# Kernel optimization log

Measured on AMD Instinct MI355X. Metric: run time of the kernel, lower is better.

## Reference

```python
import jax, jax.numpy as jnp
import numpy as np

MEMORY_SIZE = 8192
FEATURE_DIM = 512
NUM_QUERIES = 32768
EPS = 1e-12  # guard for sqrt in cdist


def setup_inputs() -> dict:
    key = jax.random.key(0)
    k1, k2, k3, k4 = jax.random.split(key, 4)
    return {
        "features": jax.random.normal(k1, (MEMORY_SIZE, FEATURE_DIM), dtype=jnp.float32),
        "positions": jax.random.normal(k2, (MEMORY_SIZE, 3), dtype=jnp.float32),
        "query_positions": jax.random.normal(k3, (NUM_QUERIES, 3), dtype=jnp.float32),
        "position_embeddings": jax.random.normal(k4, (MEMORY_SIZE, 3), dtype=jnp.float32),
    }


def _cdist(a, b):
    # Euclidean distance via ||a||^2 + ||b||^2 - 2 a.b; avoids [Q,M,3] intermediate.
    a2 = jnp.sum(a * a, axis=-1, keepdims=True)          # [Q,1]
    b2 = jnp.sum(b * b, axis=-1, keepdims=True).T        # [1,M]
    d2 = a2 + b2 - 2.0 * (a @ b.T)                       # [Q,M]
    return jnp.sqrt(jnp.maximum(d2, EPS))


def reference(features, positions, query_positions, position_embeddings):
    # --- update ---
    positions_norm = positions / jnp.linalg.norm(positions, axis=-1, keepdims=True)
    embeddings_norm = position_embeddings / jnp.linalg.norm(position_embeddings, axis=-1, keepdims=True)
    sim = positions_norm @ embeddings_norm.T             # [M,M]
    attn = jax.nn.softmax(sim, axis=-1)
    memory = attn @ features                              # [M,F]
    new_pos_emb = attn @ positions                        # [M,3]
    # --- query ---
    dist = _cdist(query_positions, new_pos_emb)           # [Q,M]
    qattn = jax.nn.softmax(-dist, axis=-1)
    retrieved = qattn @ memory                            # [Q,F]
    return retrieved
```

## Files before the change

### kernel.cpp

```cpp
#include <hip/hip_runtime.h>
#include <stdint.h>
#include <stddef.h>

#define M_SZ 8192
#define F_DIM 512
#define N_Q 32768

typedef __attribute__((ext_vector_type(4))) float f32x4;
typedef __attribute__((ext_vector_type(8))) __bf16 bf16x8;

__device__ __forceinline__ unsigned bfround_bits(float x) {
    union { float f; unsigned u; } v; v.f = x;
    return (v.u + 0x7fffu + ((v.u >> 16) & 1u)) & 0xffff0000u;
}
__device__ __forceinline__ float bits_to_f(unsigned u) {
    union { unsigned u; float f; } v; v.u = u; return v.f;
}
__device__ __forceinline__ unsigned short f2bf(float x) {
    return (unsigned short)(bfround_bits(x) >> 16);
}

__global__ void prep_kernel(const float* __restrict__ pos,
                            const float* __restrict__ emb,
                            float* __restrict__ pn4,
                            float* __restrict__ en4,
                            float* __restrict__ pos4) {
    int i = blockIdx.x * 256 + threadIdx.x;
    if (i >= M_SZ) return;
    float x = pos[i * 3 + 0], y = pos[i * 3 + 1], z = pos[i * 3 + 2];
    float inv = 1.0f / __builtin_amdgcn_sqrtf(x * x + y * y + z * z);
    pn4[i * 4 + 0] = x * inv; pn4[i * 4 + 1] = y * inv;
    pn4[i * 4 + 2] = z * inv; pn4[i * 4 + 3] = 0.0f;
    pos4[i * 4 + 0] = x; pos4[i * 4 + 1] = y;
    pos4[i * 4 + 2] = z; pos4[i * 4 + 3] = 0.0f;
    float ex = emb[i * 3 + 0], ey = emb[i * 3 + 1], ez = emb[i * 3 + 2];
    float einv = 1.0f / __builtin_amdgcn_sqrtf(ex * ex + ey * ey + ez * ez);
    en4[i * 4 + 0] = ex * einv; en4[i * 4 + 1] = ey * einv;
    en4[i * 4 + 2] = ez * einv; en4[i * 4 + 3] = 0.0f;
}

__global__ void transpose_kernel(const float* __restrict__ feat,
                                 unsigned short* __restrict__ featT) {
    __shared__ float tile[64 * 65];
    const int jb = blockIdx.x * 64, fb = blockIdx.y * 64;
    const int t = threadIdx.x;
#pragma unroll
    for (int p = 0; p < 16; ++p) {
        int idx = p * 256 + t;
        int j = idx >> 6, f = idx & 63;
        tile[j * 65 + f] = feat[(size_t)(jb + j) * F_DIM + fb + f];
    }
    __syncthreads();
#pragma unroll
    for (int p = 0; p < 16; ++p) {
        int idx = p * 256 + t;
        int f = idx >> 6, j = idx & 63;
        featT[(size_t)(fb + f) * M_SZ + jb + j] = f2bf(tile[j * 65 + f]);
    }
}

__launch_bounds__(256, 3)
__global__ void build_memory_kernel(const float* __restrict__ pn4,
                                    const float* __restrict__ en4,
                                    const float* __restrict__ pos4,
                                    const unsigned short* __restrict__ featT,
                                    unsigned short* __restrict__ memT,
                                    float* __restrict__ npe4) {
    constexpr int BM = 64, BN = 256, BK = 32;
    constexpr int PSTR = BK + 8;
    __shared__ unsigned short pbuf[BM * PSTR];
    __shared__ unsigned short vbuf[BN * PSTR];
    __shared__ f32x4 etile[BK];
    __shared__ f32x4 ptile[BK];
    __shared__ f32x4 red[256];
    __shared__ float lbuf[BM];

    const int t = threadIdx.x;
    const int lane = t & 63, wv = t >> 6;
    const int mb = blockIdx.x * BM, fb = blockIdx.y * BN;
    const int r = t & 63, jq = t >> 6;

    const f32x4 pnr = ((const f32x4*)pn4)[mb + r];

    f32x4 acc[4][4];
    const f32x4 zero4 = {0.f, 0.f, 0.f, 0.f};
#pragma unroll
    for (int m = 0; m < 4; ++m)
#pragma unroll
        for (int n = 0; n < 4; ++n) acc[m][n] = zero4;
    float nx = 0.f, ny = 0.f, nz = 0.f, lp = 0.f;

    const unsigned short* vsrc = featT + (size_t)(fb + t) * M_SZ;

    for (int kt = 0; kt < M_SZ / BK; ++kt) {
        const int jb2 = kt * BK;
        __syncthreads();
        if (t < BK) etile[t] = ((const f32x4*)en4)[jb2 + t];
        else if (t < 2 * BK) ptile[t - BK] = ((const f32x4*)pos4)[jb2 + t - BK];
        const uint4* g = (const uint4*)(vsrc + jb2);
        uint4 v0 = g[0], v1 = g[1], v2 = g[2], v3 = g[3];
        __syncthreads();

        unsigned pk[4];
#pragma unroll
        for (int i = 0; i < 8; i += 2) {
            int j = jq * 8 + i;
            f32x4 e0 = etile[j], e1 = etile[j + 1];
            float s0 = fmaf(pnr.x, e0.x, fmaf(pnr.y, e0.y, pnr.z * e0.z));
            float s1 = fmaf(pnr.x, e1.x, fmaf(pnr.y, e1.y, pnr.z * e1.z));
            unsigned b0 = bfround_bits(__builtin_amdgcn_exp2f(s0 * 1.44269504f));
            unsigned b1 = bfround_bits(__builtin_amdgcn_exp2f(s1 * 1.44269504f));
            float w0 = bits_to_f(b0), w1 = bits_to_f(b1);
            f32x4 p0 = ptile[j], p1 = ptile[j + 1];
            lp += w0 + w1;
            nx = fmaf(w0, p0.x, fmaf(w1, p1.x, nx));
            ny = fmaf(w0, p0.y, fmaf(w1, p1.y, ny));
            nz = fmaf(w0, p0.z, fmaf(w1, p1.z, nz));
            pk[i >> 1] = (b0 >> 16) | (b1 & 0xffff0000u);
        }
        *(uint4*)(pbuf + r * PSTR + jq * 8) = make_uint4(pk[0], pk[1], pk[2], pk[3]);
        uint4* vd = (uint4*)(vbuf + t * PSTR);
        vd[0] = v0; vd[1] = v1; vd[2] = v2; vd[3] = v3;
        __syncthreads();

        const int col = lane & 15, quad = lane >> 4;
        bf16x8 a[4];
#pragma unroll
        for (int m = 0; m < 4; ++m)
            a[m] = *(const bf16x8*)(pbuf + (m * 16 + col) * PSTR + quad * 8);
#pragma unroll
        for (int n = 0; n < 4; ++n) {
            bf16x8 b = *(const bf16x8*)(vbuf + ((wv * 4 + n) * 16 + col) * PSTR + quad * 8);
#pragma unroll
            for (int m = 0; m < 4; ++m)
                acc[m][n] = __builtin_amdgcn_mfma_f32_16x16x32_bf16(a[m], b, acc[m][n], 0, 0, 0);
        }
    }

    f32x4 mine = {nx, ny, nz, lp};
    red[t] = mine;
    __syncthreads();
    if (t < BM) {
        f32x4 s = red[t];
        f32x4 s1 = red[t + 64], s2 = red[t + 128], s3 = red[t + 192];
        s.x += s1.x + s2.x + s3.x;
        s.y += s1.y + s2.y + s3.y;
        s.z += s1.z + s2.z + s3.z;
        s.w += s1.w + s2.w + s3.w;
        lbuf[t] = s.w;
        if (blockIdx.y == 0) {
            float inv = 1.0f / s.w;
            float X = s.x * inv, Y = s.y * inv, Z = s.z * inv;
            f32x4 o = {X, Y, Z, X * X + Y * Y + Z * Z};
            ((f32x4*)npe4)[mb + t] = o;
        }
    }
    __syncthreads();

    const int col = lane & 15, quad = lane >> 4;
#pragma unroll
    for (int m = 0; m < 4; ++m) {
        f32x4 l4 = *(const f32x4*)(lbuf + m * 16 + quad * 4);
        f32x4 inv4 = {1.0f / l4.x, 1.0f / l4.y, 1.0f / l4.z, 1.0f / l4.w};
        int mg = mb + m * 16 + quad * 4;
#pragma unroll
        for (int n = 0; n < 4; ++n) {
            int fg = fb + (wv * 4 + n) * 16 + col;
            ushort4 o;
            o.x = f2bf(acc[m][n].x * inv4.x);
            o.y = f2bf(acc[m][n].y * inv4.y);
            o.z = f2bf(acc[m][n].z * inv4.z);
            o.w = f2bf(acc[m][n].w * inv4.w);
            *(ushort4*)(memT + (size_t)fg * M_SZ + mg) = o;
        }
    }
}

__launch_bounds__(256, 2)
__global__ void query_kernel(const float* __restrict__ qpos,
                             const float* __restrict__ npe4,
                             const unsigned short* __restrict__ memT,
                             float* __restrict__ out) {
    constexpr int BM = 128, BN = 256, BK = 32;
    constexpr int PSTR = BK + 8;
    __shared__ unsigned short pbuf[BM * PSTR];
    __shared__ unsigned short vbuf[BN * PSTR];
    __shared__ f32x4 ntile[BK];
    __shared__ float red[256];
    __shared__ float lbuf[BM];

    const int t = threadIdx.x;
    const int lane = t & 63, wv = t >> 6;
    const int qb = blockIdx.x * BM, fb = blockIdx.y * BN;
    const int r = t & 127, jh = t >> 7;

    const float qx = qpos[(size_t)(qb + r) * 3 + 0];
    const float qy = qpos[(size_t)(qb + r) * 3 + 1];
    const float qz = qpos[(size_t)(qb + r) * 3 + 2];
    const float q2 = qx * qx + qy * qy + qz * qz;

    f32x4 acc[8][4];
    const f32x4 zero4 = {0.f, 0.f, 0.f, 0.f};
#pragma unroll
    for (int m = 0; m < 8; ++m)
#pragma unroll
        for (int n = 0; n < 4; ++n) acc[m][n] = zero4;
    float lp = 0.f;

    const unsigned short* vsrc = memT + (size_t)(fb + t) * M_SZ;

    for (int kt = 0; kt < M_SZ / BK; ++kt) {
        const int jb2 = kt * BK;
        __syncthreads();
        if (t < BK) ntile[t] = ((const f32x4*)npe4)[jb2 + t];
        const uint4* g = (const uint4*)(vsrc + jb2);
        uint4 v0 = g[0], v1 = g[1], v2 = g[2], v3 = g[3];
        __syncthreads();

        unsigned pk[8];
#pragma unroll
        for (int i = 0; i < 16; i += 2) {
            int j = jh * 16 + i;
            f32x4 n0 = ntile[j], n1 = ntile[j + 1];
            float d0 = fmaf(qx, n0.x, fmaf(qy, n0.y, qz * n0.z));
            float d1 = fmaf(qx, n1.x, fmaf(qy, n1.y, qz * n1.z));
            float t0 = fmaf(-2.0f, d0, q2 + n0.w);
            float t1 = fmaf(-2.0f, d1, q2 + n1.w);
            t0 = fmaxf(t0, 1e-12f);
            t1 = fmaxf(t1, 1e-12f);
            float dd0 = __builtin_amdgcn_sqrtf(t0);
            float dd1 = __builtin_amdgcn_sqrtf(t1);
            unsigned b0 = bfround_bits(__builtin_amdgcn_exp2f(dd0 * -1.44269504f));
            unsigned b1 = bfround_bits(__builtin_amdgcn_exp2f(dd1 * -1.44269504f));
            lp += bits_to_f(b0) + bits_to_f(b1);
            pk[i >> 1] = (b0 >> 16) | (b1 & 0xffff0000u);
        }
        uint4* pd = (uint4*)(pbuf + r * PSTR + jh * 16);
        pd[0] = make_uint4(pk[0], pk[1], pk[2], pk[3]);
        pd[1] = make_uint4(pk[4], pk[5], pk[6], pk[7]);
        uint4* vd = (uint4*)(vbuf + t * PSTR);
        vd[0] = v0; vd[1] = v1; vd[2] = v2; vd[3] = v3;
        __syncthreads();

        const int col = lane & 15, quad = lane >> 4;
        bf16x8 a[8];
#pragma unroll
        for (int m = 0; m < 8; ++m)
            a[m] = *(const bf16x8*)(pbuf + (m * 16 + col) * PSTR + quad * 8);
#pragma unroll
        for (int n = 0; n < 4; ++n) {
            bf16x8 b = *(const bf16x8*)(vbuf + ((wv * 4 + n) * 16 + col) * PSTR + quad * 8);
#pragma unroll
            for (int m = 0; m < 8; ++m)
                acc[m][n] = __builtin_amdgcn_mfma_f32_16x16x32_bf16(a[m], b, acc[m][n], 0, 0, 0);
        }
    }

    red[t] = lp;
    __syncthreads();
    if (t < BM) lbuf[t] = red[t] + red[t + 128];
    __syncthreads();

    const int col = lane & 15, quad = lane >> 4;
#pragma unroll
    for (int m = 0; m < 8; ++m) {
        f32x4 l4 = *(const f32x4*)(lbuf + m * 16 + quad * 4);
        f32x4 inv4 = {1.0f / l4.x, 1.0f / l4.y, 1.0f / l4.z, 1.0f / l4.w};
        int qg = qb + m * 16 + quad * 4;
#pragma unroll
        for (int n = 0; n < 4; ++n) {
            int fg = fb + (wv * 4 + n) * 16 + col;
            out[(size_t)(qg + 0) * F_DIM + fg] = acc[m][n].x * inv4.x;
            out[(size_t)(qg + 1) * F_DIM + fg] = acc[m][n].y * inv4.y;
            out[(size_t)(qg + 2) * F_DIM + fg] = acc[m][n].z * inv4.z;
            out[(size_t)(qg + 3) * F_DIM + fg] = acc[m][n].w * inv4.w;
        }
    }
}

extern "C" void kernel_launch(void* const* d_in, const int* in_sizes, int n_in,
                              void* d_out, int out_size, void* d_ws, size_t ws_size,
                              hipStream_t stream) {
    const float* features  = (const float*)d_in[0];
    const float* positions = (const float*)d_in[1];
    const float* qpos      = (const float*)d_in[2];
    const float* pemb      = (const float*)d_in[3];
    float* out = (float*)d_out;
    char* ws = (char*)d_ws;

    unsigned short* featT = (unsigned short*)(ws);
    unsigned short* memT  = (unsigned short*)(ws + 8388608);
    float* npe4 = (float*)(ws + 16777216);
    float* pn4  = (float*)(ws + 16908288);
    float* en4  = (float*)(ws + 17039360);
    float* pos4 = (float*)(ws + 17170432);

    hipLaunchKernelGGL(prep_kernel, dim3(M_SZ / 256), dim3(256), 0, stream,
                       positions, pemb, pn4, en4, pos4);
    hipLaunchKernelGGL(transpose_kernel, dim3(M_SZ / 64, F_DIM / 64), dim3(256), 0, stream,
                       features, featT);
    hipLaunchKernelGGL(build_memory_kernel, dim3(M_SZ / 64, F_DIM / 256), dim3(256), 0, stream,
                       pn4, en4, pos4, featT, memT, npe4);
    hipLaunchKernelGGL(query_kernel, dim3(N_Q / 128, F_DIM / 256), dim3(256), 0, stream,
                       qpos, npe4, memT, out);
}
```

Measured before the change: 904.4 us.

## Retile build and query kernels to cut redundant softmax weight computation

The query kernel now covers all 512 features per block with 64 query rows, so each query's distance/exp weights are computed once rather than once per feature half. The build kernel drops to 32 rows per block so more blocks run and the grid fills the GPU better. Both kernels read the per-column vectors directly from global memory instead of staging them through shared memory, which removes one barrier per K step. Manual bf16 rounding is replaced by the compiler's native bf16 conversion. In exchange, build memory blocks repeat the feature loads more often and the query kernel keeps more accumulators in registers and uses more LDS.

```diff
diff --git a/kernel.cpp b/kernel.cpp
--- a/kernel.cpp
+++ b/kernel.cpp
@@ -8,16 +8,20 @@
 
 typedef __attribute__((ext_vector_type(4))) float f32x4;
 typedef __attribute__((ext_vector_type(8))) __bf16 bf16x8;
-
-__device__ __forceinline__ unsigned bfround_bits(float x) {
-    union { float f; unsigned u; } v; v.f = x;
-    return (v.u + 0x7fffu + ((v.u >> 16) & 1u)) & 0xffff0000u;
-}
+typedef __attribute__((ext_vector_type(2))) __bf16 bf16x2;
+
 __device__ __forceinline__ float bits_to_f(unsigned u) {
     union { unsigned u; float f; } v; v.u = u; return v.f;
 }
+__device__ __forceinline__ unsigned pk_bf16(float a, float b) {
+    union { bf16x2 v; unsigned u; } cv;
+    cv.v.x = (__bf16)a; cv.v.y = (__bf16)b;
+    return cv.u;
+}
 __device__ __forceinline__ unsigned short f2bf(float x) {
-    return (unsigned short)(bfround_bits(x) >> 16);
+    union { bf16x2 v; unsigned u; } cv;
+    cv.v.x = (__bf16)x; cv.v.y = (__bf16)0.0f;
+    return (unsigned short)(cv.u & 0xffffu);
 }
 
 __global__ void prep_kernel(const float* __restrict__ pos,
@@ -59,80 +63,79 @@
     }
 }
 
-__launch_bounds__(256, 3)
+__launch_bounds__(256, 2)
 __global__ void build_memory_kernel(const float* __restrict__ pn4,
                                     const float* __restrict__ en4,
                                     const float* __restrict__ pos4,
                                     const unsigned short* __restrict__ featT,
                                     unsigned short* __restrict__ memT,
                                     float* __restrict__ npe4) {
-    constexpr int BM = 64, BN = 256, BK = 32;
+    constexpr int BM = 32, BN = 256, BK = 32;
     constexpr int PSTR = BK + 8;
     __shared__ unsigned short pbuf[BM * PSTR];
     __shared__ unsigned short vbuf[BN * PSTR];
-    __shared__ f32x4 etile[BK];
-    __shared__ f32x4 ptile[BK];
     __shared__ f32x4 red[256];
     __shared__ float lbuf[BM];
 
     const int t = threadIdx.x;
     const int lane = t & 63, wv = t >> 6;
     const int mb = blockIdx.x * BM, fb = blockIdx.y * BN;
-    const int r = t & 63, jq = t >> 6;
+    const int r = t & 31, jq = t >> 5;
 
     const f32x4 pnr = ((const f32x4*)pn4)[mb + r];
 
-    f32x4 acc[4][4];
+    f32x4 acc[2][4];
     const f32x4 zero4 = {0.f, 0.f, 0.f, 0.f};
 #pragma unroll
-    for (int m = 0; m < 4; ++m)
+    for (int m = 0; m < 2; ++m)
 #pragma unroll
         for (int n = 0; n < 4; ++n) acc[m][n] = zero4;
     float nx = 0.f, ny = 0.f, nz = 0.f, lp = 0.f;
 
     const unsigned short* vsrc = featT + (size_t)(fb + t) * M_SZ;
+    const f32x4* en = (const f32x4*)en4;
+    const f32x4* ps = (const f32x4*)pos4;
 
     for (int kt = 0; kt < M_SZ / BK; ++kt) {
         const int jb2 = kt * BK;
-        __syncthreads();
-        if (t < BK) etile[t] = ((const f32x4*)en4)[jb2 + t];
-        else if (t < 2 * BK) ptile[t - BK] = ((const f32x4*)pos4)[jb2 + t - BK];
         const uint4* g = (const uint4*)(vsrc + jb2);
         uint4 v0 = g[0], v1 = g[1], v2 = g[2], v3 = g[3];
-        __syncthreads();
-
-        unsigned pk[4];
-#pragma unroll
-        for (int i = 0; i < 8; i += 2) {
-            int j = jq * 8 + i;
-            f32x4 e0 = etile[j], e1 = etile[j + 1];
+
+        unsigned pk2[2];
+#pragma unroll
+        for (int i = 0; i < 4; i += 2) {
+            int j = jb2 + jq * 4 + i;
+            f32x4 e0 = en[j], e1 = en[j + 1];
+            f32x4 p0 = ps[j], p1 = ps[j + 1];
             float s0 = fmaf(pnr.x, e0.x, fmaf(pnr.y, e0.y, pnr.z * e0.z));
             float s1 = fmaf(pnr.x, e1.x, fmaf(pnr.y, e1.y, pnr.z * e1.z));
-            unsigned b0 = bfround_bits(__builtin_amdgcn_exp2f(s0 * 1.44269504f));
-            unsigned b1 = bfround_bits(__builtin_amdgcn_exp2f(s1 * 1.44269504f));
-            float w0 = bits_to_f(b0), w1 = bits_to_f(b1);
-            f32x4 p0 = ptile[j], p1 = ptile[j + 1];
-            lp += w0 + w1;
-            nx = fmaf(w0, p0.x, fmaf(w1, p1.x, nx));
-            ny = fmaf(w0, p0.y, fmaf(w1, p1.y, ny));
-            nz = fmaf(w0, p0.z, fmaf(w1, p1.z, nz));
-            pk[i >> 1] = (b0 >> 16) | (b1 & 0xffff0000u);
-        }
-        *(uint4*)(pbuf + r * PSTR + jq * 8) = make_uint4(pk[0], pk[1], pk[2], pk[3]);
+            float w0 = __builtin_amdgcn_exp2f(s0 * 1.44269504f);
+            float w1 = __builtin_amdgcn_exp2f(s1 * 1.44269504f);
+            unsigned u = pk_bf16(w0, w1);
+            float w0r = bits_to_f(u << 16);
+            float w1r = bits_to_f(u & 0xffff0000u);
+            lp += w0r + w1r;
+            nx = fmaf(w0r, p0.x, fmaf(w1r, p1.x, nx));
+            ny = fmaf(w0r, p0.y, fmaf(w1r, p1.y, ny));
+            nz = fmaf(w0r, p0.z, fmaf(w1r, p1.z, nz));
+            pk2[i >> 1] = u;
+        }
+        __syncthreads();
+        *(uint2*)(pbuf + r * PSTR + jq * 4) = make_uint2(pk2[0], pk2[1]);
         uint4* vd = (uint4*)(vbuf + t * PSTR);
         vd[0] = v0; vd[1] = v1; vd[2] = v2; vd[3] = v3;
         __syncthreads();
 
         const int col = lane & 15, quad = lane >> 4;
-        bf16x8 a[4];
-#pragma unroll
-        for (int m = 0; m < 4; ++m)
+        bf16x8 a[2];
+#pragma unroll
+        for (int m = 0; m < 2; ++m)
             a[m] = *(const bf16x8*)(pbuf + (m * 16 + col) * PSTR + quad * 8);
 #pragma unroll
         for (int n = 0; n < 4; ++n) {
             bf16x8 b = *(const bf16x8*)(vbuf + ((wv * 4 + n) * 16 + col) * PSTR + quad * 8);
 #pragma unroll
-            for (int m = 0; m < 4; ++m)
+            for (int m = 0; m < 2; ++m)
                 acc[m][n] = __builtin_amdgcn_mfma_f32_16x16x32_bf16(a[m], b, acc[m][n], 0, 0, 0);
         }
     }
@@ -142,11 +145,11 @@
     __syncthreads();
     if (t < BM) {
         f32x4 s = red[t];
-        f32x4 s1 = red[t + 64], s2 = red[t + 128], s3 = red[t + 192];
-        s.x += s1.x + s2.x + s3.x;
-        s.y += s1.y + s2.y + s3.y;
-        s.z += s1.z + s2.z + s3.z;
-        s.w += s1.w + s2.w + s3.w;
+#pragma unroll
+        for (int gI = 1; gI < 8; ++gI) {
+            f32x4 o = red[t + 32 * gI];
+            s.x += o.x; s.y += o.y; s.z += o.z; s.w += o.w;
+        }
         lbuf[t] = s.w;
         if (blockIdx.y == 0) {
             float inv = 1.0f / s.w;
@@ -159,7 +162,7 @@
 
     const int col = lane & 15, quad = lane >> 4;
 #pragma unroll
-    for (int m = 0; m < 4; ++m) {
+    for (int m = 0; m < 2; ++m) {
         f32x4 l4 = *(const f32x4*)(lbuf + m * 16 + quad * 4);
         f32x4 inv4 = {1.0f / l4.x, 1.0f / l4.y, 1.0f / l4.z, 1.0f / l4.w};
         int mg = mb + m * 16 + quad * 4;
@@ -181,95 +184,94 @@
                              const float* __restrict__ npe4,
                              const unsigned short* __restrict__ memT,
                              float* __restrict__ out) {
-    constexpr int BM = 128, BN = 256, BK = 32;
+    constexpr int BM = 64, BN = 512, BK = 32;
     constexpr int PSTR = BK + 8;
     __shared__ unsigned short pbuf[BM * PSTR];
     __shared__ unsigned short vbuf[BN * PSTR];
-    __shared__ f32x4 ntile[BK];
     __shared__ float red[256];
     __shared__ float lbuf[BM];
 
     const int t = threadIdx.x;
     const int lane = t & 63, wv = t >> 6;
-    const int qb = blockIdx.x * BM, fb = blockIdx.y * BN;
-    const int r = t & 127, jh = t >> 7;
+    const int qb = blockIdx.x * BM;
+    const int r = t & 63, jq = t >> 6;
 
     const float qx = qpos[(size_t)(qb + r) * 3 + 0];
     const float qy = qpos[(size_t)(qb + r) * 3 + 1];
     const float qz = qpos[(size_t)(qb + r) * 3 + 2];
     const float q2 = qx * qx + qy * qy + qz * qz;
-
-    f32x4 acc[8][4];
+    const float m2x = -2.0f * qx, m2y = -2.0f * qy, m2z = -2.0f * qz;
+
+    f32x4 acc[4][8];
     const f32x4 zero4 = {0.f, 0.f, 0.f, 0.f};
 #pragma unroll
-    for (int m = 0; m < 8; ++m)
-#pragma unroll
-        for (int n = 0; n < 4; ++n) acc[m][n] = zero4;
+    for (int m = 0; m < 4; ++m)
+#pragma unroll
+        for (int n = 0; n < 8; ++n) acc[m][n] = zero4;
     float lp = 0.f;
 
-    const unsigned short* vsrc = memT + (size_t)(fb + t) * M_SZ;
+    const unsigned short* vsrc0 = memT + (size_t)t * M_SZ;
+    const unsigned short* vsrc1 = memT + (size_t)(t + 256) * M_SZ;
+    const f32x4* nsrc = (const f32x4*)npe4;
 
     for (int kt = 0; kt < M_SZ / BK; ++kt) {
         const int jb2 = kt * BK;
+        const uint4* g0 = (const uint4*)(vsrc0 + jb2);
+        const uint4* g1 = (const uint4*)(vsrc1 + jb2);
+        uint4 va0 = g0[0], va1 = g0[1], va2 = g0[2], va3 = g0[3];
+        uint4 vb0 = g1[0], vb1 = g1[1], vb2 = g1[2], vb3 = g1[3];
+
+        unsigned pk4[4];
+#pragma unroll
+        for (int i = 0; i < 8; i += 2) {
+            int j = jb2 + jq * 8 + i;
+            f32x4 n0 = nsrc[j], n1 = nsrc[j + 1];
+            float s0 = fmaf(m2x, n0.x, fmaf(m2y, n0.y, fmaf(m2z, n0.z, q2 + n0.w)));
+            float s1 = fmaf(m2x, n1.x, fmaf(m2y, n1.y, fmaf(m2z, n1.z, q2 + n1.w)));
+            s0 = fmaxf(s0, 1e-12f);
+            s1 = fmaxf(s1, 1e-12f);
+            float w0 = __builtin_amdgcn_exp2f(__builtin_amdgcn_sqrtf(s0) * -1.44269504f);
+            float w1 = __builtin_amdgcn_exp2f(__builtin_amdgcn_sqrtf(s1) * -1.44269504f);
+            unsigned u = pk_bf16(w0, w1);
+            lp += bits_to_f(u << 16) + bits_to_f(u & 0xffff0000u);
+            pk4[i >> 1] = u;
+        }
         __syncthreads();
-        if (t < BK) ntile[t] = ((const f32x4*)npe4)[jb2 + t];
-        const uint4* g = (const uint4*)(vsrc + jb2);
-        uint4 v0 = g[0], v1 = g[1], v2 = g[2], v3 = g[3];
+        *(uint4*)(pbuf + r * PSTR + jq * 8) = make_uint4(pk4[0], pk4[1], pk4[2], pk4[3]);
+        uint4* vd0 = (uint4*)(vbuf + t * PSTR);
+        vd0[0] = va0; vd0[1] = va1; vd0[2] = va2; vd0[3] = va3;
+        uint4* vd1 = (uint4*)(vbuf + (t + 256) * PSTR);
+        vd1[0] = vb0; vd1[1] = vb1; vd1[2] = vb2; vd1[3] = vb3;
         __syncthreads();
 
-        unsigned pk[8];
-#pragma unroll
-        for (int i = 0; i < 16; i += 2) {
-            int j = jh * 16 + i;
-            f32x4 n0 = ntile[j], n1 = ntile[j + 1];
-            float d0 = fmaf(qx, n0.x, fmaf(qy, n0.y, qz * n0.z));
-            float d1 = fmaf(qx, n1.x, fmaf(qy, n1.y, qz * n1.z));
-            float t0 = fmaf(-2.0f, d0, q2 + n0.w);
-            float t1 = fmaf(-2.0f, d1, q2 + n1.w);
-            t0 = fmaxf(t0, 1e-12f);
-            t1 = fmaxf(t1, 1e-12f);
-            float dd0 = __builtin_amdgcn_sqrtf(t0);
-            float dd1 = __builtin_amdgcn_sqrtf(t1);
-            unsigned b0 = bfround_bits(__builtin_amdgcn_exp2f(dd0 * -1.44269504f));
-            unsigned b1 = bfround_bits(__builtin_amdgcn_exp2f(dd1 * -1.44269504f));
-            lp += bits_to_f(b0) + bits_to_f(b1);
-            pk[i >> 1] = (b0 >> 16) | (b1 & 0xffff0000u);
-        }
-        uint4* pd = (uint4*)(pbuf + r * PSTR + jh * 16);
-        pd[0] = make_uint4(pk[0], pk[1], pk[2], pk[3]);
-        pd[1] = make_uint4(pk[4], pk[5], pk[6], pk[7]);
-        uint4* vd = (uint4*)(vbuf + t * PSTR);
-        vd[0] = v0; vd[1] = v1; vd[2] = v2; vd[3] = v3;
-        __syncthreads();
-
         const int col = lane & 15, quad = lane >> 4;
-        bf16x8 a[8];
-#pragma unroll
-        for (int m = 0; m < 8; ++m)
+        bf16x8 a[4];
+#pragma unroll
+        for (int m = 0; m < 4; ++m)
             a[m] = *(const bf16x8*)(pbuf + (m * 16 + col) * PSTR + quad * 8);
 #pragma unroll
-        for (int n = 0; n < 4; ++n) {
-            bf16x8 b = *(const bf16x8*)(vbuf + ((wv * 4 + n) * 16 + col) * PSTR + quad * 8);
-#pragma unroll
-            for (int m = 0; m < 8; ++m)
+        for (int n = 0; n < 8; ++n) {
+            bf16x8 b = *(const bf16x8*)(vbuf + ((wv * 8 + n) * 16 + col) * PSTR + quad * 8);
+#pragma unroll
+            for (int m = 0; m < 4; ++m)
                 acc[m][n] = __builtin_amdgcn_mfma_f32_16x16x32_bf16(a[m], b, acc[m][n], 0, 0, 0);
         }
     }
 
     red[t] = lp;
     __syncthreads();
-    if (t < BM) lbuf[t] = red[t] + red[t + 128];
+    if (t < BM) lbuf[t] = red[t] + red[t + 64] + red[t + 128] + red[t + 192];
     __syncthreads();
 
     const int col = lane & 15, quad = lane >> 4;
 #pragma unroll
-    for (int m = 0; m < 8; ++m) {
+    for (int m = 0; m < 4; ++m) {
         f32x4 l4 = *(const f32x4*)(lbuf + m * 16 + quad * 4);
         f32x4 inv4 = {1.0f / l4.x, 1.0f / l4.y, 1.0f / l4.z, 1.0f / l4.w};
         int qg = qb + m * 16 + quad * 4;
 #pragma unroll
-        for (int n = 0; n < 4; ++n) {
-            int fg = fb + (wv * 4 + n) * 16 + col;
+        for (int n = 0; n < 8; ++n) {
+            int fg = (wv * 8 + n) * 16 + col;
             out[(size_t)(qg + 0) * F_DIM + fg] = acc[m][n].x * inv4.x;
             out[(size_t)(qg + 1) * F_DIM + fg] = acc[m][n].y * inv4.y;
             out[(size_t)(qg + 2) * F_DIM + fg] = acc[m][n].z * inv4.z;
@@ -299,8 +301,8 @@
                        positions, pemb, pn4, en4, pos4);
     hipLaunchKernelGGL(transpose_kernel, dim3(M_SZ / 64, F_DIM / 64), dim3(256), 0, stream,
                        features, featT);
-    hipLaunchKernelGGL(build_memory_kernel, dim3(M_SZ / 64, F_DIM / 256), dim3(256), 0, stream,
+    hipLaunchKernelGGL(build_memory_kernel, dim3(M_SZ / 32, F_DIM / 256), dim3(256), 0, stream,
                        pn4, en4, pos4, featT, memT, npe4);
-    hipLaunchKernelGGL(query_kernel, dim3(N_Q / 128, F_DIM / 256), dim3(256), 0, stream,
+    hipLaunchKernelGGL(query_kernel, dim3(N_Q / 64), dim3(256), 0, stream,
                        qpos, npe4, memT, out);
 }
```

Measured after the change: 1.057 ms. 1.17x slower.
